# Performance work log

Hardware: AMD Instinct MI355X
Metric: run time of the kernel (lower is better)

The kernel has to match this reference:

```python
import jax, jax.numpy as jnp
import numpy as np

R, K = 16, 64  # rel_size (heads), key_size (head dim)
LN_EPS = 1e-5


def apply_rope(x, pos):
    # pos: [B,S,1,K], halves are sin/cos; x: [B,S,R,K]
    sin, cos = jnp.split(pos, 2, axis=-1)
    x0, x1 = jnp.split(x, 2, axis=-1)
    return jnp.concatenate([x0 * cos - x1 * sin, x0 * sin + x1 * cos], axis=-1)


def setup_inputs() -> dict:
    key = jax.random.key(0)
    ks = jax.random.split(key, 6)
    B, S, H = 2, 2048, 1024
    x = jax.random.normal(ks[0], (B, S, H), dtype=jnp.float32)
    pos = jax.random.uniform(ks[1], (B, S, 1, K), dtype=jnp.float32)
    W_qkv = jax.random.normal(ks[2], (H, R * K * 3), dtype=jnp.float32) * (H ** -0.5)
    b_qkv = jax.random.normal(ks[3], (R * K * 3,), dtype=jnp.float32) * 0.02
    W_out = jax.random.normal(ks[4], (R * K, H), dtype=jnp.float32) * ((R * K) ** -0.5)
    b_out = jax.random.normal(ks[5], (H,), dtype=jnp.float32) * 0.02
    ln_g = jnp.ones((H,), dtype=jnp.float32)
    ln_b = jnp.zeros((H,), dtype=jnp.float32)
    return {"x": x, "pos": pos, "W_qkv": W_qkv, "b_qkv": b_qkv,
            "W_out": W_out, "b_out": b_out, "ln_g": ln_g, "ln_b": ln_b}


def reference(x, pos, W_qkv, b_qkv, W_out, b_out, ln_g, ln_b):
    B, S, H = x.shape
    qkv = (x @ W_qkv + b_qkv).reshape(B, S, R, 3 * K)
    q, k, v = jnp.split(qkv, 3, axis=-1)  # each [B,S,R,K]
    k = k / jnp.linalg.norm(k, axis=-1, keepdims=True)
    q = apply_rope(q, pos)
    k = apply_rope(k, pos)
    # SDPA with scale=1 (as in the original call)
    scores = jnp.einsum('bqhd,bkhd->bhqk', q, k)
    attn = jax.nn.softmax(scores, axis=-1)
    ctx = jnp.einsum('bhqk,bkhd->bqhd', attn, v).reshape(B, S, R * K)
    postx = ctx @ W_out + b_out
    y = x + postx
    mu = jnp.mean(y, axis=-1, keepdims=True)
    var = jnp.mean(jnp.square(y - mu), axis=-1, keepdims=True)
    return (y - mu) * jax.lax.rsqrt(var + LN_EPS) * ln_g + ln_b
```

## Files before the change

### kernel.cpp

```cpp
#include <hip/hip_runtime.h>


#define B_   2
#define S_   2048
#define H_   1024
#define R_   16
#define BS_  (B_*S_)
#define NQKV 3072
#define LOG2E 1.44269504088896f

typedef float    floatx4 __attribute__((ext_vector_type(4)));
typedef _Float16 half8   __attribute__((ext_vector_type(8)));
typedef _Float16 half4   __attribute__((ext_vector_type(4)));
typedef __fp16   fp16x2  __attribute__((ext_vector_type(2)));

#if __has_builtin(__builtin_amdgcn_exp2f)
#define EXP2(x) __builtin_amdgcn_exp2f(x)
#else
#define EXP2(x) exp2f(x)
#endif

__device__ __forceinline__ void gl_lds16(const _Float16* g, _Float16* l) {
    __builtin_amdgcn_global_load_lds(
        (const __attribute__((address_space(1))) unsigned int*)g,
        (__attribute__((address_space(3))) unsigned int*)l, 16, 0, 0);
}

__global__ __launch_bounds__(256) void prep0_kernel(
    const float* __restrict__ x, _Float16* __restrict__ x_h,
    const float* __restrict__ W_qkv, _Float16* __restrict__ wqkv_t,
    const float* __restrict__ W_out, _Float16* __restrict__ wout_t)
{
    __shared__ float tile[32][33];
    int bid = blockIdx.x, tid = threadIdx.x;
    if (bid < 4096) {
        int i = bid * 1024 + tid * 4;
        float4 v = *(const float4*)(x + i);
        half4 h;
        h.x = (_Float16)v.x; h.y = (_Float16)v.y;
        h.z = (_Float16)v.z; h.w = (_Float16)v.w;
        *(half4*)(x_h + i) = h;
        return;
    }
    const float* in; _Float16* out; int rows, cols, bx, by;
    if (bid < 7168) {
        int t = bid - 4096;
        in = W_qkv; out = wqkv_t; rows = H_; cols = NQKV;
        bx = t % 96; by = t / 96;
    } else {
        int t = bid - 7168;
        in = W_out; out = wout_t; rows = H_; cols = H_;
        bx = t & 31; by = t >> 5;
    }
    int cx = bx * 32, ry = by * 32;
    int tx = tid & 31, ty = tid >> 5;
#pragma unroll
    for (int i = 0; i < 32; i += 8)
        tile[ty + i][tx] = in[(size_t)(ry + ty + i) * cols + cx + tx];
    __syncthreads();
#pragma unroll
    for (int i = 0; i < 32; i += 8)
        out[(size_t)(cx + ty + i) * rows + ry + tx] = (_Float16)tile[tx][ty + i];
}

__global__ __launch_bounds__(256) void gemm_f16_mfma(
    const _Float16* __restrict__ A, const _Float16* __restrict__ Bt,
    const float* __restrict__ bias, _Float16* __restrict__ Ch,
    int M, int N, int Kd)
{
    __shared__ _Float16 Als[2][4096];
    __shared__ _Float16 Bls[2][4096];
    int tid  = threadIdx.x;
    int lane = tid & 63, w = tid >> 6;
    int wr = w >> 1, wc = w & 1;
    int fr = lane & 15, fq = lane >> 4;
    int m0 = blockIdx.y * 128, n0 = blockIdx.x * 128;

    floatx4 acc[4][4] = {};

    const _Float16* ga[2]; const _Float16* gb[2];
    int loff[2];
#pragma unroll
    for (int i2 = 0; i2 < 2; ++i2) {
        int ch = 2 * w + i2;
        int row = ch * 16 + (lane >> 2), col = (lane & 3) * 8;
        ga[i2] = A  + (size_t)(m0 + row) * Kd + col;
        gb[i2] = Bt + (size_t)(n0 + row) * Kd + col;
        loff[i2] = ch * 512;
    }

    int nIter = Kd >> 5;
#pragma unroll
    for (int i2 = 0; i2 < 2; ++i2) {
        gl_lds16(ga[i2], &Als[0][loff[i2]]);
        gl_lds16(gb[i2], &Bls[0][loff[i2]]);
    }

    for (int it = 0; it < nIter; ++it) {
        int cur = it & 1;
        __syncthreads();
        if (it + 1 < nIter) {
            int k1 = (it + 1) << 5;
#pragma unroll
            for (int i2 = 0; i2 < 2; ++i2) {
                gl_lds16(ga[i2] + k1, &Als[cur ^ 1][loff[i2]]);
                gl_lds16(gb[i2] + k1, &Bls[cur ^ 1][loff[i2]]);
            }
        }
        const _Float16* Ab = Als[cur];
        const _Float16* Bb = Bls[cur];
        half8 af[4], bf[4];
#pragma unroll
        for (int i = 0; i < 4; ++i)
            af[i] = *(const half8*)(Ab + (wr * 64 + i * 16 + fr) * 32 + fq * 8);
#pragma unroll
        for (int j = 0; j < 4; ++j)
            bf[j] = *(const half8*)(Bb + (wc * 64 + j * 16 + fr) * 32 + fq * 8);
#pragma unroll
        for (int i = 0; i < 4; ++i)
#pragma unroll
            for (int j = 0; j < 4; ++j)
                acc[i][j] = __builtin_amdgcn_mfma_f32_16x16x32_f16(
                    af[i], bf[j], acc[i][j], 0, 0, 0);
    }

#pragma unroll
    for (int i = 0; i < 4; ++i)
#pragma unroll
        for (int j = 0; j < 4; ++j)
#pragma unroll
            for (int r2 = 0; r2 < 4; ++r2) {
                int row = m0 + wr * 64 + i * 16 + fq * 4 + r2;
                int col = n0 + wc * 64 + j * 16 + fr;
                Ch[(size_t)row * N + col] = (_Float16)(acc[i][j][r2] + bias[col]);
            }
}

__global__ __launch_bounds__(256) void gemm64_f16_mfma(
    const _Float16* __restrict__ A, const _Float16* __restrict__ Bt,
    const float* __restrict__ bias, const float* __restrict__ resid,
    float* __restrict__ Cf, int M, int N, int Kd)
{
    __shared__ _Float16 Als[2][2048];
    __shared__ _Float16 Bls[2][2048];
    int tid = threadIdx.x, lane = tid & 63, w = tid >> 6;
    int wr = w >> 1, wc = w & 1;
    int fr = lane & 15, fq = lane >> 4;
    int m0 = blockIdx.y * 64, n0 = blockIdx.x * 64;

    floatx4 acc[2][2] = {};

    int srow = w * 16 + (lane >> 2), scol = (lane & 3) * 8;
    const _Float16* ga = A  + (size_t)(m0 + srow) * Kd + scol;
    const _Float16* gb = Bt + (size_t)(n0 + srow) * Kd + scol;
    int loff = w * 512;

    int nIter = Kd >> 5;
    gl_lds16(ga, &Als[0][loff]);
    gl_lds16(gb, &Bls[0][loff]);

    for (int it = 0; it < nIter; ++it) {
        int cur = it & 1;
        __syncthreads();
        if (it + 1 < nIter) {
            int k1 = (it + 1) << 5;
            gl_lds16(ga + k1, &Als[cur ^ 1][loff]);
            gl_lds16(gb + k1, &Bls[cur ^ 1][loff]);
        }
        const _Float16* Ab = Als[cur];
        const _Float16* Bb = Bls[cur];
        half8 af[2], bf[2];
#pragma unroll
        for (int i = 0; i < 2; ++i)
            af[i] = *(const half8*)(Ab + (wr * 32 + i * 16 + fr) * 32 + fq * 8);
#pragma unroll
        for (int j = 0; j < 2; ++j)
            bf[j] = *(const half8*)(Bb + (wc * 32 + j * 16 + fr) * 32 + fq * 8);
#pragma unroll
        for (int i = 0; i < 2; ++i)
#pragma unroll
            for (int j = 0; j < 2; ++j)
                acc[i][j] = __builtin_amdgcn_mfma_f32_16x16x32_f16(
                    af[i], bf[j], acc[i][j], 0, 0, 0);
    }

#pragma unroll
    for (int i = 0; i < 2; ++i)
#pragma unroll
        for (int j = 0; j < 2; ++j)
#pragma unroll
            for (int r2 = 0; r2 < 4; ++r2) {
                int row = m0 + wr * 32 + i * 16 + fq * 4 + r2;
                int col = n0 + wc * 32 + j * 16 + fr;
                Cf[(size_t)row * N + col] =
                    acc[i][j][r2] + bias[col] + resid[(size_t)row * N + col];
            }
}

__global__ __launch_bounds__(256) void prep1_kernel(
    const _Float16* __restrict__ qkvh, const float* __restrict__ pos,
    _Float16* __restrict__ qt, _Float16* __restrict__ kt,
    _Float16* __restrict__ vt2)
{
    __shared__ float tile[64][65];
    int head = blockIdx.x, tau = blockIdx.y;
    int s0 = tau * 64;
    int b = head >> 4, rh = head & 15;
    int lane = threadIdx.x & 63, w = threadIdx.x >> 6;

#pragma unroll
    for (int si = w; si < 64; si += 4)
        tile[si][lane] =
            (float)qkvh[(size_t)(b * S_ + s0 + si) * NQKV + rh * 192 + 128 + lane];
    __syncthreads();
    {
        int P = lane;
        int op = P >> 3;
        int hi = (P >> 2) & 1, lo = P & 3;
#pragma unroll
        for (int d = w; d < 64; d += 4) {
            int ol = op ^ (d & 7);
            int key = 32 * (ol >> 2) + 16 * hi + 4 * (ol & 3) + lo;
            vt2[(((size_t)head * 32 + tau) * 64 + d) * 64 + P] = (_Float16)tile[key][d];
        }
    }

    for (int i = 0; i < 16; ++i) {
        int s = s0 + w * 16 + i;
        int bs = b * S_ + s;
        const _Float16* base = qkvh + (size_t)bs * NQKV + rh * 192;
        float qv = (float)base[lane];
        float kv = (float)base[64 + lane];

        float ss = kv * kv;
#pragma unroll
        for (int off = 32; off > 0; off >>= 1) ss += __shfl_xor(ss, off);
        kv *= rsqrtf(ss);

        int j = lane & 31;
        float sn = pos[(size_t)bs * 64 + j];
        float cs = pos[(size_t)bs * 64 + 32 + j];
        float qp = __shfl_xor(qv, 32);
        float kp = __shfl_xor(kv, 32);
        float qo, ko;
        if (lane < 32) { qo = qv * cs - qp * sn; ko = kv * cs - kp * sn; }
        else           { qo = qp * sn + qv * cs; ko = kp * sn + kv * cs; }

        size_t oidx = ((size_t)head * S_ + s) * 64 + lane;
        qt[oidx] = (_Float16)(qo * LOG2E);
        kt[oidx] = (_Float16)ko;
    }
}

__global__ __launch_bounds__(256) void attn_mfma_kernel(
    const _Float16* __restrict__ qt, const _Float16* __restrict__ kt,
    const _Float16* __restrict__ vt2,
    _Float16* __restrict__ opart, float* __restrict__ lpart)
{
    __shared__ _Float16 Kls[2][4096];
    __shared__ _Float16 Vls[2][4096];

    int head = blockIdx.x, q0 = blockIdx.y * 128, ks = blockIdx.z;
    int b = head >> 4, rh = head & 15;
    int tid = threadIdx.x, lane = tid & 63, w = tid >> 6;
    int g = lane >> 4, c = lane & 15;

    half8 qf[2][2];
    float mL[2], l_s[2] = {0.f, 0.f};
#pragma unroll
    for (int qg = 0; qg < 2; ++qg) {
        const _Float16* qp =
            qt + ((size_t)head * S_ + q0 + w * 32 + qg * 16 + c) * 64 + 8 * g;
        qf[qg][0] = *(const half8*)qp;
        qf[qg][1] = *(const half8*)(qp + 32);
        float qq = 0.f;
#pragma unroll
        for (int i = 0; i < 8; ++i) {
            float a = (float)qf[qg][0][i], b2 = (float)qf[qg][1][i];
            qq += a * a + b2 * b2;
        }
        qq += __shfl_xor(qq, 16);
        qq += __shfl_xor(qq, 32);
        mL[qg] = sqrtf(qq);
    }

    floatx4 o_acc[2][4] = {};

    const _Float16* kg[2]; const _Float16* vg[2];
    int loff[2];
#pragma unroll
    for (int i2 = 0; i2 < 2; ++i2) {
        int ch = 2 * w + i2;
        int krow = ch * 8 + (lane >> 3);
        int koct = (lane & 7) ^ (lane >> 3);
        kg[i2] = kt + ((size_t)head * S_ + krow) * 64 + koct * 8;
        vg[i2] = vt2 + ((size_t)head * 32) * 4096 + ch * 512 + lane * 8;
        loff[i2] = ch * 512;
    }

    int co = c & 7;
    int jbase = ks << 4;

#pragma unroll
    for (int i2 = 0; i2 < 2; ++i2) {
        gl_lds16(kg[i2] + (size_t)jbase * 4096, &Kls[0][loff[i2]]);
        gl_lds16(vg[i2] + (size_t)jbase * 4096, &Vls[0][loff[i2]]);
    }

    for (int jt = 0; jt < 16; ++jt) {
        int cur = jt & 1;
        __syncthreads();
        if (jt + 1 < 16) {
            size_t joff = (size_t)(jbase + jt + 1) * 4096;
#pragma unroll
            for (int i2 = 0; i2 < 2; ++i2) {
                gl_lds16(kg[i2] + joff, &Kls[cur ^ 1][loff[i2]]);
                gl_lds16(vg[i2] + joff, &Vls[cur ^ 1][loff[i2]]);
            }
        }
        const _Float16* Kbuf = Kls[cur];
        const _Float16* Vbuf = Vls[cur];

        half8 kfr[8];
#pragma unroll
        for (int t = 0; t < 4; ++t) {
            const _Float16* krow = Kbuf + (16 * t + c) * 64;
            kfr[2 * t]     = *(const half8*)(krow + ((g) ^ co) * 8);
            kfr[2 * t + 1] = *(const half8*)(krow + ((4 + g) ^ co) * 8);
        }

        union { half8 v; fp16x2 h2[4]; } pf[2][2];
#pragma unroll
        for (int qg = 0; qg < 2; ++qg) {
            floatx4 sacc[4];
#pragma unroll
            for (int t = 0; t < 4; ++t) {
                floatx4 z = {};
                z = __builtin_amdgcn_mfma_f32_16x16x32_f16(
                    kfr[2 * t], qf[qg][0], z, 0, 0, 0);
                z = __builtin_amdgcn_mfma_f32_16x16x32_f16(
                    kfr[2 * t + 1], qf[qg][1], z, 0, 0, 0);
                sacc[t] = z;
            }
            float mLq = mL[qg], ps = 0.f;
#pragma unroll
            for (int t = 0; t < 4; ++t)
#pragma unroll
                for (int r = 0; r < 4; ++r) {
                    float p = EXP2(sacc[t][r] - mLq);
                    sacc[t][r] = p;
                    ps += p;
                }
            l_s[qg] += ps;
            pf[qg][0].h2[0] = __builtin_amdgcn_cvt_pkrtz(sacc[0][0], sacc[0][1]);
            pf[qg][0].h2[1] = __builtin_amdgcn_cvt_pkrtz(sacc[0][2], sacc[0][3]);
            pf[qg][0].h2[2] = __builtin_amdgcn_cvt_pkrtz(sacc[1][0], sacc[1][1]);
            pf[qg][0].h2[3] = __builtin_amdgcn_cvt_pkrtz(sacc[1][2], sacc[1][3]);
            pf[qg][1].h2[0] = __builtin_amdgcn_cvt_pkrtz(sacc[2][0], sacc[2][1]);
            pf[qg][1].h2[1] = __builtin_amdgcn_cvt_pkrtz(sacc[2][2], sacc[2][3]);
            pf[qg][1].h2[2] = __builtin_amdgcn_cvt_pkrtz(sacc[3][0], sacc[3][1]);
            pf[qg][1].h2[3] = __builtin_amdgcn_cvt_pkrtz(sacc[3][2], sacc[3][3]);
        }

#pragma unroll
        for (int t = 0; t < 4; ++t) {
            const _Float16* vrow = Vbuf + (16 * t + c) * 64;
            half8 v0 = *(const half8*)(vrow + ((g) ^ co) * 8);
            half8 v1 = *(const half8*)(vrow + ((4 + g) ^ co) * 8);
#pragma unroll
            for (int qg = 0; qg < 2; ++qg) {
                o_acc[qg][t] = __builtin_amdgcn_mfma_f32_16x16x32_f16(
                    v0, pf[qg][0].v, o_acc[qg][t], 0, 0, 0);
                o_acc[qg][t] = __builtin_amdgcn_mfma_f32_16x16x32_f16(
                    v1, pf[qg][1].v, o_acc[qg][t], 0, 0, 0);
            }
        }
    }

#pragma unroll
    for (int qg = 0; qg < 2; ++qg) {
        float lt = l_s[qg];
        lt += __shfl_xor(lt, 16);
        lt += __shfl_xor(lt, 32);
        int q = q0 + w * 32 + qg * 16 + c;
        if (lane < 16)
            lpart[((size_t)ks * 32 + head) * S_ + q] = lt;
        size_t rowbase =
            ((size_t)ks * BS_ + (size_t)(b * S_ + q)) * 1024 + rh * 64;
#pragma unroll
        for (int t = 0; t < 4; ++t) {
            union { half4 v; fp16x2 h2[2]; } e;
            e.h2[0] = __builtin_amdgcn_cvt_pkrtz(o_acc[qg][t][0], o_acc[qg][t][1]);
            e.h2[1] = __builtin_amdgcn_cvt_pkrtz(o_acc[qg][t][2], o_acc[qg][t][3]);
            *(half4*)(opart + rowbase + 16 * t + 4 * g) = e.v;
        }
    }
}

__global__ __launch_bounds__(256) void merge_kernel(
    const _Float16* __restrict__ opart, const float* __restrict__ lpart,
    _Float16* __restrict__ ctx)
{
    int idx = blockIdx.x * 256 + threadIdx.x;
    int row = idx >> 7;
    int col = (idx & 127) * 8;
    int b = row >> 11, s = row & 2047;
    int head = b * 16 + (col >> 6);
    float l0 = lpart[(size_t)head * S_ + s];
    float l1 = lpart[(size_t)(32 + head) * S_ + s];
    float inv = 1.f / (l0 + l1);
    size_t off = (size_t)row * 1024 + col;
    half8 a = *(const half8*)(opart + off);
    half8 b8 = *(const half8*)(opart + (size_t)BS_ * 1024 + off);
    union { half8 v; fp16x2 h2[4]; } e;
#pragma unroll
    for (int i = 0; i < 4; ++i)
        e.h2[i] = __builtin_amdgcn_cvt_pkrtz(
            ((float)a[2 * i]     + (float)b8[2 * i])     * inv,
            ((float)a[2 * i + 1] + (float)b8[2 * i + 1]) * inv);
    *(half8*)(ctx + off) = e.v;
}

__global__ __launch_bounds__(256) void ln_kernel(
    float* __restrict__ y, const float* __restrict__ g, const float* __restrict__ bb)
{
    int row = blockIdx.x, tid = threadIdx.x;
    float* p = y + (size_t)row * 1024;
    float4 v = ((const float4*)p)[tid];
    float sum = v.x + v.y + v.z + v.w;
    float sq  = v.x*v.x + v.y*v.y + v.z*v.z + v.w*v.w;
#pragma unroll
    for (int off = 32; off > 0; off >>= 1) {
        sum += __shfl_xor(sum, off);
        sq  += __shfl_xor(sq,  off);
    }
    __shared__ float rs[4], rq[4];
    int w = tid >> 6;
    if ((tid & 63) == 0) { rs[w] = sum; rq[w] = sq; }
    __syncthreads();
    sum = rs[0] + rs[1] + rs[2] + rs[3];
    sq  = rq[0] + rq[1] + rq[2] + rq[3];
    float mean = sum * (1.f / 1024.f);
    float var  = sq * (1.f / 1024.f) - mean * mean;
    float inv  = rsqrtf(var + 1e-5f);
    float4 gv = ((const float4*)g)[tid];
    float4 bv = ((const float4*)bb)[tid];
    v.x = (v.x - mean) * inv * gv.x + bv.x;
    v.y = (v.y - mean) * inv * gv.y + bv.y;
    v.z = (v.z - mean) * inv * gv.z + bv.z;
    v.w = (v.w - mean) * inv * gv.w + bv.w;
    ((float4*)p)[tid] = v;
}

extern "C" void kernel_launch(void* const* d_in, const int* in_sizes, int n_in,
                              void* d_out, int out_size, void* d_ws, size_t ws_size,
                              hipStream_t stream)
{
    const float* x     = (const float*)d_in[0];
    const float* pos   = (const float*)d_in[1];
    const float* W_qkv = (const float*)d_in[2];
    const float* b_qkv = (const float*)d_in[3];
    const float* W_out = (const float*)d_in[4];
    const float* b_out = (const float*)d_in[5];
    const float* ln_g  = (const float*)d_in[6];
    const float* ln_b  = (const float*)d_in[7];
    float* out = (float*)d_out;

    char* ws = (char*)d_ws;
    _Float16* x_h    = (_Float16*)(ws);
    _Float16* wqkv_t = (_Float16*)(ws + ((size_t)8  << 20));
    _Float16* wout_t = (_Float16*)(ws + ((size_t)14 << 20));
    _Float16* qkvh   = (_Float16*)(ws + ((size_t)16 << 20));
    _Float16* qt_h   = (_Float16*)(ws + ((size_t)40 << 20));
    _Float16* kt_h   = (_Float16*)(ws + ((size_t)48 << 20));
    _Float16* vt2_h  = (_Float16*)(ws + ((size_t)56 << 20));
    _Float16* ctx_h  = (_Float16*)(ws + ((size_t)64 << 20));
    _Float16* opart  = (_Float16*)(ws + ((size_t)72 << 20));
    float*    lpart  = (float*)   (ws + ((size_t)88 << 20));

    prep0_kernel<<<8192, 256, 0, stream>>>(x, x_h, W_qkv, wqkv_t, W_out, wout_t);

    gemm_f16_mfma<<<dim3(NQKV / 128, BS_ / 128), 256, 0, stream>>>(
        x_h, wqkv_t, b_qkv, qkvh, BS_, NQKV, H_);

    prep1_kernel<<<dim3(32, 32), 256, 0, stream>>>(qkvh, pos, qt_h, kt_h, vt2_h);

    attn_mfma_kernel<<<dim3(32, 16, 2), 256, 0, stream>>>(
        qt_h, kt_h, vt2_h, opart, lpart);

    merge_kernel<<<2048, 256, 0, stream>>>(opart, lpart, ctx_h);

    gemm64_f16_mfma<<<dim3(H_ / 64, BS_ / 64), 256, 0, stream>>>(
        ctx_h, wout_t, b_out, x, out, BS_, H_, H_);

    ln_kernel<<<BS_, 256, 0, stream>>>(out, ln_g, ln_b);
}
```

Baseline: 223.9 us.

## Split attention keys four ways and drop LDS double buffering

Raises the key-dimension split of the attention kernel from 2 to 4, so each block walks 8 key tiles instead of 16 and the grid is twice as large. The K/V LDS double buffer becomes a single buffer with load-then-sync each iteration, cutting LDS use per block to allow more resident blocks. The merge kernel now sums four partial outputs and denominators, and the lpart workspace moves to fit the larger opart. The cost is no overlap of global-to-LDS loads with compute inside a block, plus extra partial-output traffic in the merge.

```diff
diff --git a/kernel.cpp b/kernel.cpp
--- a/kernel.cpp
+++ b/kernel.cpp
@@ -8,6 +8,7 @@
 #define BS_  (B_*S_)
 #define NQKV 3072
 #define LOG2E 1.44269504088896f
+#define KSPL 4
 
 typedef float    floatx4 __attribute__((ext_vector_type(4)));
 typedef _Float16 half8   __attribute__((ext_vector_type(8)));
@@ -257,8 +258,8 @@
     const _Float16* __restrict__ vt2,
     _Float16* __restrict__ opart, float* __restrict__ lpart)
 {
-    __shared__ _Float16 Kls[2][4096];
-    __shared__ _Float16 Vls[2][4096];
+    __shared__ _Float16 Kls[4096];
+    __shared__ _Float16 Vls[4096];
 
     int head = blockIdx.x, q0 = blockIdx.y * 128, ks = blockIdx.z;
     int b = head >> 4, rh = head & 15;
@@ -287,44 +288,35 @@
     floatx4 o_acc[2][4] = {};
 
     const _Float16* kg[2]; const _Float16* vg[2];
-    int loff[2];
+    _Float16 *kl_[2], *vl_[2];
 #pragma unroll
     for (int i2 = 0; i2 < 2; ++i2) {
         int ch = 2 * w + i2;
         int krow = ch * 8 + (lane >> 3);
         int koct = (lane & 7) ^ (lane >> 3);
         kg[i2] = kt + ((size_t)head * S_ + krow) * 64 + koct * 8;
+        kl_[i2] = Kls + ch * 512;
         vg[i2] = vt2 + ((size_t)head * 32) * 4096 + ch * 512 + lane * 8;
-        loff[i2] = ch * 512;
+        vl_[i2] = Vls + ch * 512;
     }
 
     int co = c & 7;
-    int jbase = ks << 4;
-
-#pragma unroll
-    for (int i2 = 0; i2 < 2; ++i2) {
-        gl_lds16(kg[i2] + (size_t)jbase * 4096, &Kls[0][loff[i2]]);
-        gl_lds16(vg[i2] + (size_t)jbase * 4096, &Vls[0][loff[i2]]);
-    }
-
-    for (int jt = 0; jt < 16; ++jt) {
-        int cur = jt & 1;
+    int jbase = ks * 8;
+
+    for (int jt = 0; jt < 8; ++jt) {
+        size_t joff = (size_t)(jbase + jt) * 4096;
         __syncthreads();
-        if (jt + 1 < 16) {
-            size_t joff = (size_t)(jbase + jt + 1) * 4096;
-#pragma unroll
-            for (int i2 = 0; i2 < 2; ++i2) {
-                gl_lds16(kg[i2] + joff, &Kls[cur ^ 1][loff[i2]]);
-                gl_lds16(vg[i2] + joff, &Vls[cur ^ 1][loff[i2]]);
-            }
-        }
-        const _Float16* Kbuf = Kls[cur];
-        const _Float16* Vbuf = Vls[cur];
+#pragma unroll
+        for (int i2 = 0; i2 < 2; ++i2) {
+            gl_lds16(kg[i2] + joff, kl_[i2]);
+            gl_lds16(vg[i2] + joff, vl_[i2]);
+        }
+        __syncthreads();
 
         half8 kfr[8];
 #pragma unroll
         for (int t = 0; t < 4; ++t) {
-            const _Float16* krow = Kbuf + (16 * t + c) * 64;
+            const _Float16* krow = Kls + (16 * t + c) * 64;
             kfr[2 * t]     = *(const half8*)(krow + ((g) ^ co) * 8);
             kfr[2 * t + 1] = *(const half8*)(krow + ((4 + g) ^ co) * 8);
         }
@@ -364,7 +356,7 @@
 
 #pragma unroll
         for (int t = 0; t < 4; ++t) {
-            const _Float16* vrow = Vbuf + (16 * t + c) * 64;
+            const _Float16* vrow = Vls + (16 * t + c) * 64;
             half8 v0 = *(const half8*)(vrow + ((g) ^ co) * 8);
             half8 v1 = *(const half8*)(vrow + ((4 + g) ^ co) * 8);
 #pragma unroll
@@ -406,18 +398,23 @@
     int col = (idx & 127) * 8;
     int b = row >> 11, s = row & 2047;
     int head = b * 16 + (col >> 6);
-    float l0 = lpart[(size_t)head * S_ + s];
-    float l1 = lpart[(size_t)(32 + head) * S_ + s];
-    float inv = 1.f / (l0 + l1);
+    float lsum = 0.f;
+#pragma unroll
+    for (int ks = 0; ks < KSPL; ++ks)
+        lsum += lpart[((size_t)ks * 32 + head) * S_ + s];
+    float inv = 1.f / lsum;
     size_t off = (size_t)row * 1024 + col;
-    half8 a = *(const half8*)(opart + off);
-    half8 b8 = *(const half8*)(opart + (size_t)BS_ * 1024 + off);
+    float o[8] = {};
+#pragma unroll
+    for (int ks = 0; ks < KSPL; ++ks) {
+        half8 a = *(const half8*)(opart + (size_t)ks * BS_ * 1024 + off);
+#pragma unroll
+        for (int i = 0; i < 8; ++i) o[i] += (float)a[i];
+    }
     union { half8 v; fp16x2 h2[4]; } e;
 #pragma unroll
     for (int i = 0; i < 4; ++i)
-        e.h2[i] = __builtin_amdgcn_cvt_pkrtz(
-            ((float)a[2 * i]     + (float)b8[2 * i])     * inv,
-            ((float)a[2 * i + 1] + (float)b8[2 * i + 1]) * inv);
+        e.h2[i] = __builtin_amdgcn_cvt_pkrtz(o[2 * i] * inv, o[2 * i + 1] * inv);
     *(half8*)(ctx + off) = e.v;
 }
 
@@ -476,7 +473,7 @@
     _Float16* vt2_h  = (_Float16*)(ws + ((size_t)56 << 20));
     _Float16* ctx_h  = (_Float16*)(ws + ((size_t)64 << 20));
     _Float16* opart  = (_Float16*)(ws + ((size_t)72 << 20));
-    float*    lpart  = (float*)   (ws + ((size_t)88 << 20));
+    float*    lpart  = (float*)   (ws + ((size_t)104 << 20));
 
     prep0_kernel<<<8192, 256, 0, stream>>>(x, x_h, W_qkv, wqkv_t, W_out, wout_t);
 
@@ -485,7 +482,7 @@
 
     prep1_kernel<<<dim3(32, 32), 256, 0, stream>>>(qkvh, pos, qt_h, kt_h, vt2_h);
 
-    attn_mfma_kernel<<<dim3(32, 16, 2), 256, 0, stream>>>(
+    attn_mfma_kernel<<<dim3(32, 16, KSPL), 256, 0, stream>>>(
         qt_h, kt_h, vt2_h, opart, lpart);
 
     merge_kernel<<<2048, 256, 0, stream>>>(opart, lpart, ctx_h);
```

New measurement: 229.3 us. 2.4% more time.
